# Kernel tuning notes

Measured on AMD Instinct MI355X. Metric: run time of the kernel, lower is better.

The kernel has to match this reference:

```python
import jax, jax.numpy as jnp
import numpy as np

N_NODES = 100000
N_EDGES = 600000
IN_C, HID, OUT_C = 128, 128, 64
DROPOUT_P = 0.5
BN_EPS = 1e-5


def setup_inputs() -> dict:
    key = jax.random.key(0)
    ks = jax.random.split(key, 16)
    d = {}
    d["x"] = jax.random.normal(ks[0], (N_NODES, IN_C), dtype=jnp.float32)
    d["edge_index"] = jax.random.randint(ks[1], (2, N_EDGES), 0, N_NODES, dtype=jnp.int32)
    d["norm_A"] = jax.random.uniform(ks[2], (N_EDGES,), dtype=jnp.float32)
    # GCNConv weights (glorot-ish scale) and biases
    d["W1"] = jax.random.normal(ks[3], (IN_C, HID), dtype=jnp.float32) / np.sqrt(IN_C)
    d["b1"] = jnp.zeros((HID,), dtype=jnp.float32)
    d["W2"] = jax.random.normal(ks[4], (HID, HID), dtype=jnp.float32) / np.sqrt(HID)
    d["b2"] = jnp.zeros((HID,), dtype=jnp.float32)
    d["W3"] = jax.random.normal(ks[5], (HID, HID), dtype=jnp.float32) / np.sqrt(HID)
    d["b3"] = jnp.zeros((HID,), dtype=jnp.float32)
    # BatchNorm affine params (2 BN layers for num_layers=3)
    d["g1"] = jnp.ones((HID,), dtype=jnp.float32)
    d["bt1"] = jnp.zeros((HID,), dtype=jnp.float32)
    d["g2"] = jnp.ones((HID,), dtype=jnp.float32)
    d["bt2"] = jnp.zeros((HID,), dtype=jnp.float32)
    # final projection (jk_type='max' -> Linear(HID, OUT_C))
    d["Wf"] = jax.random.normal(ks[6], (HID, OUT_C), dtype=jnp.float32) / np.sqrt(HID)
    d["bf"] = jnp.zeros((OUT_C,), dtype=jnp.float32)
    return d


def _gcn_conv(h, edge_index, ew, W, b):
    # GCNConv(cached=False, normalize=False): transform then weighted scatter-add
    h = h @ W                                   # [N, C]
    msg = ew[:, None] * h[edge_index[0]]        # gather sources, scale per-edge
    agg = jax.ops.segment_sum(msg, edge_index[1], num_segments=N_NODES)
    return agg + b


def _bn_train(h, g, bt):
    mu = jnp.mean(h, axis=0)
    var = jnp.var(h, axis=0)  # biased, as torch BN uses for normalization
    return g * (h - mu) * jax.lax.rsqrt(var + BN_EPS) + bt


def _dropout(h, key):
    keep = jax.random.bernoulli(key, 1.0 - DROPOUT_P, h.shape)
    return jnp.where(keep, h / (1.0 - DROPOUT_P), 0.0)


def reference(x, edge_index, norm_A, W1, b1, W2, b2, W3, b3, g1, bt1, g2, bt2, Wf, bf):
    dk = jax.random.key(42)
    k1, k2 = jax.random.split(dk)
    # layer 1
    h = _gcn_conv(x, edge_index, norm_A, W1, b1)
    h = jax.nn.relu(_bn_train(h, g1, bt1))
    x1 = h
    h = _dropout(h, k1)
    # layer 2
    h = _gcn_conv(h, edge_index, norm_A, W2, b2)
    h = jax.nn.relu(_bn_train(h, g2, bt2))
    x2 = h
    h = _dropout(h, k2)
    # layer 3 (no BN/relu/dropout)
    x3 = _gcn_conv(h, edge_index, norm_A, W3, b3)
    # JumpingKnowledge 'max': elementwise max over layer outputs
    jk = jnp.maximum(jnp.maximum(x1, x2), x3)
    out = jk @ Wf + bf
    return jax.nn.log_softmax(out, axis=1)
```

## Files before the change

kernel.cpp:

```cpp
#include <hip/hip_runtime.h>
#include <stdint.h>

#define N_NODES 100000
#define N_EDGES 600000
#define HID 128
#define OUT_C 64
#define NELEMS 12800000
#define BN_EPS 1e-5f
#define LP 136

typedef short bf16x8 __attribute__((ext_vector_type(8)));
typedef float f32x4 __attribute__((ext_vector_type(4)));

__device__ __forceinline__ unsigned short f2bf(float f) {
  uint32_t u = __float_as_uint(f);
  uint32_t r = u + 0x7FFFu + ((u >> 16) & 1u);
  return (unsigned short)(r >> 16);
}
__device__ __forceinline__ float bf_lo(uint32_t u) { return __uint_as_float(u << 16); }
__device__ __forceinline__ float bf_hi(uint32_t u) { return __uint_as_float(u & 0xFFFF0000u); }

__device__ __host__ __forceinline__ void threefry2x32(uint32_t k0, uint32_t k1,
                                                      uint32_t x0, uint32_t x1,
                                                      uint32_t& o0, uint32_t& o1) {
  uint32_t ks0 = k0, ks1 = k1, ks2 = k0 ^ k1 ^ 0x1BD11BDAu;
  x0 += ks0; x1 += ks1;
#define TFR(r) { x0 += x1; x1 = (x1 << (r)) | (x1 >> (32 - (r))); x1 ^= x0; }
  TFR(13) TFR(15) TFR(26) TFR(6)
  x0 += ks1; x1 += ks2 + 1u;
  TFR(17) TFR(29) TFR(16) TFR(24)
  x0 += ks2; x1 += ks0 + 2u;
  TFR(13) TFR(15) TFR(26) TFR(6)
  x0 += ks0; x1 += ks1 + 3u;
  TFR(17) TFR(29) TFR(16) TFR(24)
  x0 += ks1; x1 += ks2 + 4u;
  TFR(13) TFR(15) TFR(26) TFR(6)
  x0 += ks2; x1 += ks0 + 5u;
#undef TFR
  o0 = x0; o1 = x1;
}

__device__ __forceinline__ uint32_t jax_bits32(uint32_t k0, uint32_t k1, uint32_t i) {
  uint32_t b0, b1;
  threefry2x32(k0, k1, 0u, i, b0, b1);
  return b0 ^ b1;
}

__global__ __launch_bounds__(256) void transpose_w(const float* __restrict__ W,
                                                   int K, int C,
                                                   unsigned short* __restrict__ out) {
  int idx = blockIdx.x * 256 + threadIdx.x;
  if (idx < K * C) {
    int k = idx / C, c = idx - k * C;
    out[c * K + k] = f2bf(W[idx]);
  }
}

__device__ __forceinline__ void stage_Wt(const float* __restrict__ W,
                                         unsigned short* Wt, int tid) {
#pragma unroll
  for (int i = 0; i < 16; ++i) {
    int f4 = tid + i * 256;
    int k = f4 >> 5;
    int cq = f4 & 31;
    float4 w = *(const float4*)(W + k * 128 + cq * 4);
    Wt[(cq * 4 + 0) * LP + k] = f2bf(w.x);
    Wt[(cq * 4 + 1) * LP + k] = f2bf(w.y);
    Wt[(cq * 4 + 2) * LP + k] = f2bf(w.z);
    Wt[(cq * 4 + 3) * LP + k] = f2bf(w.w);
  }
}

__device__ __forceinline__ void mfma_compute_store(const unsigned short* At,
                                                   const unsigned short* Wt,
                                                   unsigned short* __restrict__ O,
                                                   int rbase, int tid) {
  const int lane = tid & 63;
  const int wv = tid >> 6;
  const int m = lane & 15;
  const int kg = lane >> 4;
  f32x4 acc0 = {0,0,0,0}, acc1 = {0,0,0,0}, acc2 = {0,0,0,0}, acc3 = {0,0,0,0};
  f32x4 acc4 = {0,0,0,0}, acc5 = {0,0,0,0}, acc6 = {0,0,0,0}, acc7 = {0,0,0,0};
  const unsigned short* Arow = At + (wv * 16 + m) * LP;
#pragma unroll
  for (int ks = 0; ks < 4; ++ks) {
    bf16x8 af = *(const bf16x8*)(Arow + ks * 32 + kg * 8);
#define MF(n, accn) { bf16x8 bfr = *(const bf16x8*)(Wt + (n * 16 + m) * LP + ks * 32 + kg * 8); \
    accn = __builtin_amdgcn_mfma_f32_16x16x32_bf16(af, bfr, accn, 0, 0, 0); }
    MF(0, acc0) MF(1, acc1) MF(2, acc2) MF(3, acc3)
    MF(4, acc4) MF(5, acc5) MF(6, acc6) MF(7, acc7)
#undef MF
  }
#define ST(n, accn) {                                                       \
  _Pragma("unroll")                                                         \
  for (int j = 0; j < 4; ++j) {                                             \
    int grow = rbase + wv * 16 + kg * 4 + j;                                \
    if (grow < N_NODES) O[(size_t)grow * 128 + n * 16 + m] = f2bf(accn[j]); \
  } }
  ST(0, acc0) ST(1, acc1) ST(2, acc2) ST(3, acc3)
  ST(4, acc4) ST(5, acc5) ST(6, acc6) ST(7, acc7)
#undef ST
}

__global__ __launch_bounds__(256) void gemm_mfma(const float* __restrict__ A,
                                                 const float* __restrict__ W,
                                                 unsigned short* __restrict__ O) {
  __shared__ __align__(16) unsigned short Wt[128 * LP];
  __shared__ __align__(16) unsigned short At[64 * LP];
  const int tid = threadIdx.x;
  const int rbase = blockIdx.x * 64;
  stage_Wt(W, Wt, tid);
#pragma unroll
  for (int i = 0; i < 8; ++i) {
    int f4 = tid + i * 256;
    int r = f4 >> 5;
    int cq = f4 & 31;
    int grow = rbase + r;
    if (grow >= N_NODES) grow = N_NODES - 1;
    float4 a = *(const float4*)(A + (size_t)grow * 128 + cq * 4);
    uint32_t p0 = (uint32_t)f2bf(a.x) | ((uint32_t)f2bf(a.y) << 16);
    uint32_t p1 = (uint32_t)f2bf(a.z) | ((uint32_t)f2bf(a.w) << 16);
    *(uint2*)(At + r * LP + cq * 4) = make_uint2(p0, p1);
  }
  __syncthreads();
  mfma_compute_store(At, Wt, O, rbase, tid);
}

__global__ __launch_bounds__(256) void gemm_mfma_fused(const float* __restrict__ AGG,
                                                       const float2* __restrict__ ss,
                                                       const unsigned short* __restrict__ Wt,
                                                       unsigned int* __restrict__ Xb,
                                                       unsigned short* __restrict__ O,
                                                       uint32_t k0, uint32_t k1) {
  const int tid = threadIdx.x;
  const int lane = tid & 63;
  const int wv = tid >> 6;
  const int m = lane & 15;
  const int kg = lane >> 4;
  const int rbase = blockIdx.x * 64;
  int row = rbase + wv * 16 + m;
  bool valid = row < N_NODES;
  int rowc = valid ? row : N_NODES - 1;
  const float* Ar = AGG + (size_t)rowc * 128 + kg * 8;
  bf16x8 af0, af1, af2, af3;
#define LDF(ksc, afk) {                                                        \
    float4 a0 = *(const float4*)(Ar + ksc);                                    \
    float4 a1 = *(const float4*)(Ar + ksc + 4);                                \
    const float2* ssp = ss + ksc + kg * 8;                                     \
    float av[8] = {a0.x, a0.y, a0.z, a0.w, a1.x, a1.y, a1.z, a1.w};            \
    unsigned short yb[8];                                                      \
    _Pragma("unroll")                                                          \
    for (int jj = 0; jj < 8; ++jj) {                                           \
      float2 sv = ssp[jj];                                                     \
      float yv = fmaxf(fmaf(av[jj], sv.x, sv.y), 0.f);                         \
      uint32_t bits = jax_bits32(k0, k1, (uint32_t)(rowc * 128 + ksc + kg * 8 + jj)); \
      yb[jj] = f2bf(yv);                                                       \
      afk[jj] = (short)f2bf((bits & 0x80000000u) ? 0.f : 2.f * yv);            \
    }                                                                          \
    if (valid) {                                                               \
      uint4 yp;                                                                \
      yp.x = (uint32_t)yb[0] | ((uint32_t)yb[1] << 16);                        \
      yp.y = (uint32_t)yb[2] | ((uint32_t)yb[3] << 16);                        \
      yp.z = (uint32_t)yb[4] | ((uint32_t)yb[5] << 16);                        \
      yp.w = (uint32_t)yb[6] | ((uint32_t)yb[7] << 16);                        \
      *(uint4*)(Xb + (size_t)row * 64 + (ksc) / 2 + kg * 4) = yp;              \
    } }
  LDF(0, af0) LDF(32, af1) LDF(64, af2) LDF(96, af3)
#undef LDF
  f32x4 acc0 = {0,0,0,0}, acc1 = {0,0,0,0}, acc2 = {0,0,0,0}, acc3 = {0,0,0,0};
  f32x4 acc4 = {0,0,0,0}, acc5 = {0,0,0,0}, acc6 = {0,0,0,0}, acc7 = {0,0,0,0};
  const unsigned short* Wm = Wt + m * 128 + kg * 8;
#define MFMA_ALL(afk, ksc)                                                              \
  acc0 = __builtin_amdgcn_mfma_f32_16x16x32_bf16(afk, *(const bf16x8*)(Wm + 0 * 2048 + ksc), acc0, 0, 0, 0); \
  acc1 = __builtin_amdgcn_mfma_f32_16x16x32_bf16(afk, *(const bf16x8*)(Wm + 1 * 2048 + ksc), acc1, 0, 0, 0); \
  acc2 = __builtin_amdgcn_mfma_f32_16x16x32_bf16(afk, *(const bf16x8*)(Wm + 2 * 2048 + ksc), acc2, 0, 0, 0); \
  acc3 = __builtin_amdgcn_mfma_f32_16x16x32_bf16(afk, *(const bf16x8*)(Wm + 3 * 2048 + ksc), acc3, 0, 0, 0); \
  acc4 = __builtin_amdgcn_mfma_f32_16x16x32_bf16(afk, *(const bf16x8*)(Wm + 4 * 2048 + ksc), acc4, 0, 0, 0); \
  acc5 = __builtin_amdgcn_mfma_f32_16x16x32_bf16(afk, *(const bf16x8*)(Wm + 5 * 2048 + ksc), acc5, 0, 0, 0); \
  acc6 = __builtin_amdgcn_mfma_f32_16x16x32_bf16(afk, *(const bf16x8*)(Wm + 6 * 2048 + ksc), acc6, 0, 0, 0); \
  acc7 = __builtin_amdgcn_mfma_f32_16x16x32_bf16(afk, *(const bf16x8*)(Wm + 7 * 2048 + ksc), acc7, 0, 0, 0);
  MFMA_ALL(af0, 0) MFMA_ALL(af1, 32) MFMA_ALL(af2, 64) MFMA_ALL(af3, 96)
#undef MFMA_ALL
#pragma unroll
  for (int j = 0; j < 4; ++j) {
    int orow = rbase + wv * 16 + kg * 4 + j;
    if (orow < N_NODES) {
      unsigned short* op = O + (size_t)orow * 128 + m;
      op[0 * 16] = f2bf(acc0[j]); op[1 * 16] = f2bf(acc1[j]);
      op[2 * 16] = f2bf(acc2[j]); op[3 * 16] = f2bf(acc3[j]);
      op[4 * 16] = f2bf(acc4[j]); op[5 * 16] = f2bf(acc5[j]);
      op[6 * 16] = f2bf(acc6[j]); op[7 * 16] = f2bf(acc7[j]);
    }
  }
}

__global__ __launch_bounds__(256) void csr_count(const int* __restrict__ ei,
                                                 int* __restrict__ cnt) {
  int e = blockIdx.x * 256 + threadIdx.x;
  if (e < N_EDGES) atomicAdd(&cnt[ei[e + N_EDGES]], 1);
}

__global__ __launch_bounds__(256) void scan_blocks(int* __restrict__ cnt,
                                                   int* __restrict__ bsum) {
  __shared__ int tmp[256];
  int tid = threadIdx.x;
  int i = blockIdx.x * 256 + tid;
  int v = (i < N_NODES) ? cnt[i] : 0;
  tmp[tid] = v;
  __syncthreads();
  for (int off = 1; off < 256; off <<= 1) {
    int t = (tid >= off) ? tmp[tid - off] : 0;
    __syncthreads();
    if (tid >= off) tmp[tid] += t;
    __syncthreads();
  }
  if (i < N_NODES) cnt[i] = tmp[tid] - v;
  if (tid == 255) bsum[blockIdx.x] = tmp[255];
}

__global__ __launch_bounds__(512) void scan_bsum(int* __restrict__ bsum, int nb) {
  __shared__ int tmp[512];
  int tid = threadIdx.x;
  int v = (tid < nb) ? bsum[tid] : 0;
  tmp[tid] = v;
  __syncthreads();
  for (int off = 1; off < 512; off <<= 1) {
    int t = (tid >= off) ? tmp[tid - off] : 0;
    __syncthreads();
    if (tid >= off) tmp[tid] += t;
    __syncthreads();
  }
  if (tid < nb) bsum[tid] = tmp[tid] - v;
}

__global__ __launch_bounds__(256) void add_offsets(int* __restrict__ cnt,
                                                   const int* __restrict__ bsum,
                                                   int* __restrict__ row_ptr) {
  int i = blockIdx.x * 256 + threadIdx.x;
  if (i < N_NODES) {
    int r = cnt[i] + bsum[blockIdx.x];
    row_ptr[i] = r;
    cnt[i] = r;
  }
  if (i == 0) row_ptr[N_NODES] = N_EDGES;
}

__global__ __launch_bounds__(256) void csr_fill(const int* __restrict__ ei,
                                                const float* __restrict__ ew,
                                                int* __restrict__ cursor,
                                                int2* __restrict__ edges) {
  int e = blockIdx.x * 256 + threadIdx.x;
  if (e < N_EDGES) {
    int d = ei[e + N_EDGES];
    int p = atomicAdd(&cursor[d], 1);
    edges[p] = make_int2(ei[e], __float_as_int(ew[e]));
  }
}

template <bool STATS>
__global__ __launch_bounds__(256) void gather_agg(const unsigned int* __restrict__ Hb,
                                                  const int* __restrict__ row_ptr,
                                                  const int2* __restrict__ edges,
                                                  const float* __restrict__ bias,
                                                  float* __restrict__ AGG,
                                                  float* __restrict__ partials) {
  const int hw = threadIdx.x >> 5;
  const int l32 = threadIdx.x & 31;
  const int node = blockIdx.x * 8 + hw;
  float4 acc = *(const float4*)(bias + l32 * 4);
  const int beg = row_ptr[node];
  const int end = row_ptr[node + 1];
  const unsigned int* Hp = Hb + l32 * 2;
  int j = beg;
  for (; j + 3 < end; j += 4) {
    int2 e0 = edges[j + 0];
    int2 e1 = edges[j + 1];
    int2 e2 = edges[j + 2];
    int2 e3 = edges[j + 3];
    uint2 u0 = *(const uint2*)(Hp + (size_t)e0.x * 64);
    uint2 u1 = *(const uint2*)(Hp + (size_t)e1.x * 64);
    uint2 u2 = *(const uint2*)(Hp + (size_t)e2.x * 64);
    uint2 u3 = *(const uint2*)(Hp + (size_t)e3.x * 64);
    float w0 = __int_as_float(e0.y), w1 = __int_as_float(e1.y);
    float w2 = __int_as_float(e2.y), w3 = __int_as_float(e3.y);
    acc.x += w0 * bf_lo(u0.x) + w1 * bf_lo(u1.x) + w2 * bf_lo(u2.x) + w3 * bf_lo(u3.x);
    acc.y += w0 * bf_hi(u0.x) + w1 * bf_hi(u1.x) + w2 * bf_hi(u2.x) + w3 * bf_hi(u3.x);
    acc.z += w0 * bf_lo(u0.y) + w1 * bf_lo(u1.y) + w2 * bf_lo(u2.y) + w3 * bf_lo(u3.y);
    acc.w += w0 * bf_hi(u0.y) + w1 * bf_hi(u1.y) + w2 * bf_hi(u2.y) + w3 * bf_hi(u3.y);
  }
  for (; j < end; ++j) {
    int2 e = edges[j];
    uint2 u = *(const uint2*)(Hp + (size_t)e.x * 64);
    float w = __int_as_float(e.y);
    acc.x += w * bf_lo(u.x);
    acc.y += w * bf_hi(u.x);
    acc.z += w * bf_lo(u.y);
    acc.w += w * bf_hi(u.y);
  }
  *(float4*)(AGG + (size_t)node * 128 + l32 * 4) = acc;

  if (STATS) {
    __shared__ float st[8][256];
    st[hw][l32 * 4 + 0] = acc.x;
    st[hw][l32 * 4 + 1] = acc.y;
    st[hw][l32 * 4 + 2] = acc.z;
    st[hw][l32 * 4 + 3] = acc.w;
    st[hw][128 + l32 * 4 + 0] = acc.x * acc.x;
    st[hw][128 + l32 * 4 + 1] = acc.y * acc.y;
    st[hw][128 + l32 * 4 + 2] = acc.z * acc.z;
    st[hw][128 + l32 * 4 + 3] = acc.w * acc.w;
    __syncthreads();
    float t = 0.f;
#pragma unroll
    for (int g = 0; g < 8; ++g) t += st[g][threadIdx.x];
    unsafeAtomicAdd(&partials[(blockIdx.x & 63) * 256 + threadIdx.x], t);
  }
}

__global__ __launch_bounds__(128) void stats_finalize(float* __restrict__ partials,
                                                      const float* __restrict__ g,
                                                      const float* __restrict__ bt,
                                                      float2* __restrict__ ss) {
  int c = threadIdx.x;
  float s = 0.f, q = 0.f;
#pragma unroll 8
  for (int b = 0; b < 64; ++b) {
    s += partials[b * 256 + c];
    q += partials[b * 256 + 128 + c];
  }
#pragma unroll 8
  for (int b = 0; b < 64; ++b) {
    partials[b * 256 + c] = 0.f;
    partials[b * 256 + 128 + c] = 0.f;
  }
  float mu = s * (1.0f / N_NODES);
  float var = fmaxf(q * (1.0f / N_NODES) - mu * mu, 0.f);
  float inv = rsqrtf(var + BN_EPS);
  float sc = g[c] * inv;
  ss[c] = make_float2(sc, bt[c] - mu * sc);
}

__global__ __launch_bounds__(256) void jk_final_mfma(const unsigned int* __restrict__ X1b,
                                                     const unsigned int* __restrict__ X2b,
                                                     const float* __restrict__ X3,
                                                     const float* __restrict__ Wf,
                                                     const float* __restrict__ bf,
                                                     float* __restrict__ OUT) {
  __shared__ __align__(16) unsigned short Wt[64 * LP];
  __shared__ __align__(16) unsigned short At[64 * LP];
  const int tid = threadIdx.x;
  const int rbase = blockIdx.x * 64;
#pragma unroll
  for (int i = 0; i < 8; ++i) {
    int f4 = tid + i * 256;
    int k = f4 >> 4;
    int cq = f4 & 15;
    float4 w = *(const float4*)(Wf + k * 64 + cq * 4);
    Wt[(cq * 4 + 0) * LP + k] = f2bf(w.x);
    Wt[(cq * 4 + 1) * LP + k] = f2bf(w.y);
    Wt[(cq * 4 + 2) * LP + k] = f2bf(w.z);
    Wt[(cq * 4 + 3) * LP + k] = f2bf(w.w);
  }
#pragma unroll
  for (int i = 0; i < 8; ++i) {
    int f4 = tid + i * 256;
    int r = f4 >> 5;
    int cq = f4 & 31;
    int grow = rbase + r;
    if (grow >= N_NODES) grow = N_NODES - 1;
    uint2 u1 = *(const uint2*)(X1b + (size_t)grow * 64 + cq * 2);
    uint2 u2 = *(const uint2*)(X2b + (size_t)grow * 64 + cq * 2);
    float4 x3 = *(const float4*)(X3 + (size_t)grow * 128 + cq * 4);
    float m0 = fmaxf(fmaxf(bf_lo(u1.x), bf_lo(u2.x)), x3.x);
    float m1 = fmaxf(fmaxf(bf_hi(u1.x), bf_hi(u2.x)), x3.y);
    float m2 = fmaxf(fmaxf(bf_lo(u1.y), bf_lo(u2.y)), x3.z);
    float m3 = fmaxf(fmaxf(bf_hi(u1.y), bf_hi(u2.y)), x3.w);
    uint32_t p0 = (uint32_t)f2bf(m0) | ((uint32_t)f2bf(m1) << 16);
    uint32_t p1 = (uint32_t)f2bf(m2) | ((uint32_t)f2bf(m3) << 16);
    *(uint2*)(At + r * LP + cq * 4) = make_uint2(p0, p1);
  }
  __syncthreads();
  const int lane = tid & 63;
  const int wv = tid >> 6;
  const int m = lane & 15;
  const int kg = lane >> 4;
  f32x4 acc0 = {0,0,0,0}, acc1 = {0,0,0,0}, acc2 = {0,0,0,0}, acc3 = {0,0,0,0};
  const unsigned short* Arow = At + (wv * 16 + m) * LP;
#pragma unroll
  for (int ks = 0; ks < 4; ++ks) {
    bf16x8 af = *(const bf16x8*)(Arow + ks * 32 + kg * 8);
#define MF(n, accn) { bf16x8 bfr = *(const bf16x8*)(Wt + (n * 16 + m) * LP + ks * 32 + kg * 8); \
    accn = __builtin_amdgcn_mfma_f32_16x16x32_bf16(af, bfr, accn, 0, 0, 0); }
    MF(0, acc0) MF(1, acc1) MF(2, acc2) MF(3, acc3)
#undef MF
  }
  float bf0 = bf[m], bf1 = bf[16 + m], bf2 = bf[32 + m], bf3 = bf[48 + m];
#pragma unroll
  for (int j = 0; j < 4; ++j) {
    int row = rbase + wv * 16 + kg * 4 + j;
    float v0 = acc0[j] + bf0;
    float v1 = acc1[j] + bf1;
    float v2 = acc2[j] + bf2;
    float v3 = acc3[j] + bf3;
    float M = fmaxf(fmaxf(v0, v1), fmaxf(v2, v3));
#pragma unroll
    for (int s = 1; s < 16; s <<= 1) M = fmaxf(M, __shfl_xor(M, s));
    float sum = expf(v0 - M) + expf(v1 - M) + expf(v2 - M) + expf(v3 - M);
#pragma unroll
    for (int s = 1; s < 16; s <<= 1) sum += __shfl_xor(sum, s);
    float ls = M + logf(sum);
    if (row < N_NODES) {
      float* o = OUT + (size_t)row * 64;
      o[m] = v0 - ls;
      o[16 + m] = v1 - ls;
      o[32 + m] = v2 - ls;
      o[48 + m] = v3 - ls;
    }
  }
}

extern "C" void kernel_launch(void* const* d_in, const int* in_sizes, int n_in,
                              void* d_out, int out_size, void* d_ws, size_t ws_size,
                              hipStream_t stream) {
  const float* x   = (const float*)d_in[0];
  const int*   ei  = (const int*)d_in[1];
  const float* ew  = (const float*)d_in[2];
  const float* W1  = (const float*)d_in[3];
  const float* b1  = (const float*)d_in[4];
  const float* W2  = (const float*)d_in[5];
  const float* b2  = (const float*)d_in[6];
  const float* W3  = (const float*)d_in[7];
  const float* b3  = (const float*)d_in[8];
  const float* g1  = (const float*)d_in[9];
  const float* bt1 = (const float*)d_in[10];
  const float* g2  = (const float*)d_in[11];
  const float* bt2 = (const float*)d_in[12];
  const float* Wf  = (const float*)d_in[13];
  const float* bfb = (const float*)d_in[14];
  float* out = (float*)d_out;

  float* B0 = (float*)d_ws;
  float* B1 = B0 + NELEMS;
  float* B2 = B1 + NELEMS;
  float* B3 = B2 + NELEMS;
  int2* edges = (int2*)(B3 + NELEMS);
  int* cursor = (int*)(edges + N_EDGES);
  int* row_ptr = cursor + N_NODES;
  int* bsum = row_ptr + N_NODES + 1;
  float* partials = (float*)(bsum + 512);
  float2* ss1 = (float2*)(partials + 64 * 256);
  float2* ss2 = ss1 + 128;
  unsigned short* Wt2 = (unsigned short*)(ss2 + 128);
  unsigned short* Wt3 = Wt2 + 128 * 128;
  unsigned short* P = (unsigned short*)B0;
  unsigned int* Pu = (unsigned int*)B0;
  unsigned int* X1b = (unsigned int*)B2;
  unsigned int* X2b = (unsigned int*)B3;

  uint32_t k1_0, k1_1, k2_0, k2_1;
  threefry2x32(0u, 42u, 0u, 0u, k1_0, k1_1);
  threefry2x32(0u, 42u, 0u, 1u, k2_0, k2_1);

  const int GEMM_GRID = (N_NODES + 63) / 64;
  const int EDGE_GRID = (N_EDGES + 255) / 256;
  const int NODE_GRID = (N_NODES + 255) / 256;
  const int AGG_GRID  = N_NODES / 8;
  const int FINAL_GRID = (N_NODES + 63) / 64;
  const int TR_GRID = (128 * 128 + 255) / 256;

  transpose_w<<<TR_GRID, 256, 0, stream>>>(W2, 128, 128, Wt2);
  transpose_w<<<TR_GRID, 256, 0, stream>>>(W3, 128, 128, Wt3);
  hipMemsetAsync(cursor, 0, N_NODES * sizeof(int), stream);
  hipMemsetAsync(partials, 0, 64 * 256 * sizeof(float), stream);
  csr_count<<<EDGE_GRID, 256, 0, stream>>>(ei, cursor);
  scan_blocks<<<NODE_GRID, 256, 0, stream>>>(cursor, bsum);
  scan_bsum<<<1, 512, 0, stream>>>(bsum, NODE_GRID);
  add_offsets<<<NODE_GRID, 256, 0, stream>>>(cursor, bsum, row_ptr);
  csr_fill<<<EDGE_GRID, 256, 0, stream>>>(ei, ew, cursor, edges);

  gemm_mfma<<<GEMM_GRID, 256, 0, stream>>>(x, W1, P);
  gather_agg<true><<<AGG_GRID, 256, 0, stream>>>(Pu, row_ptr, edges, b1, B1, partials);
  stats_finalize<<<1, 128, 0, stream>>>(partials, g1, bt1, ss1);
  gemm_mfma_fused<<<GEMM_GRID, 256, 0, stream>>>(B1, ss1, Wt2, X1b, P, k1_0, k1_1);
  gather_agg<true><<<AGG_GRID, 256, 0, stream>>>(Pu, row_ptr, edges, b2, B1, partials);
  stats_finalize<<<1, 128, 0, stream>>>(partials, g2, bt2, ss2);
  gemm_mfma_fused<<<GEMM_GRID, 256, 0, stream>>>(B1, ss2, Wt3, X2b, P, k2_0, k2_1);
  gather_agg<false><<<AGG_GRID, 256, 0, stream>>>(Pu, row_ptr, edges, b3, B1, nullptr);
  jk_final_mfma<<<FINAL_GRID, 256, 0, stream>>>(X1b, X2b, B1, Wf, bfb, out);
}
```

Before: 352.7 us.

## Fold BN stats finalize into fused GEMM and store layer-3 aggregate as bf16

```diff
diff --git a/kernel.cpp b/kernel.cpp
--- a/kernel.cpp
+++ b/kernel.cpp
@@ -46,14 +46,16 @@
   return b0 ^ b1;
 }
 
-__global__ __launch_bounds__(256) void transpose_w(const float* __restrict__ W,
-                                                   int K, int C,
-                                                   unsigned short* __restrict__ out) {
+__global__ __launch_bounds__(256) void transpose_w23(const float* __restrict__ W2,
+                                                     const float* __restrict__ W3,
+                                                     unsigned short* __restrict__ Wt2,
+                                                     unsigned short* __restrict__ Wt3) {
   int idx = blockIdx.x * 256 + threadIdx.x;
-  if (idx < K * C) {
-    int k = idx / C, c = idx - k * C;
-    out[c * K + k] = f2bf(W[idx]);
-  }
+  const float* W = (idx < 16384) ? W2 : W3;
+  unsigned short* out = (idx < 16384) ? Wt2 : Wt3;
+  int e = idx & 16383;
+  int k = e >> 7, c = e & 127;
+  out[c * 128 + k] = f2bf(W[e]);
 }
 
 __device__ __forceinline__ void stage_Wt(const float* __restrict__ W,
@@ -127,12 +129,32 @@
 }
 
 __global__ __launch_bounds__(256) void gemm_mfma_fused(const float* __restrict__ AGG,
-                                                       const float2* __restrict__ ss,
+                                                       const float* __restrict__ partials,
+                                                       const float* __restrict__ g,
+                                                       const float* __restrict__ bt,
                                                        const unsigned short* __restrict__ Wt,
                                                        unsigned int* __restrict__ Xb,
                                                        unsigned short* __restrict__ O,
                                                        uint32_t k0, uint32_t k1) {
   const int tid = threadIdx.x;
+  __shared__ float red[256];
+  __shared__ float2 ssl[128];
+  {
+    float t0 = 0.f;
+#pragma unroll 8
+    for (int b = 0; b < 64; ++b) t0 += partials[b * 256 + tid];
+    red[tid] = t0;
+    __syncthreads();
+    if (tid < 128) {
+      float s = red[tid], q = red[128 + tid];
+      float mu = s * (1.0f / N_NODES);
+      float var = fmaxf(q * (1.0f / N_NODES) - mu * mu, 0.f);
+      float inv = rsqrtf(var + BN_EPS);
+      float sc = g[tid] * inv;
+      ssl[tid] = make_float2(sc, bt[tid] - mu * sc);
+    }
+    __syncthreads();
+  }
   const int lane = tid & 63;
   const int wv = tid >> 6;
   const int m = lane & 15;
@@ -146,7 +168,7 @@
 #define LDF(ksc, afk) {                                                        \
     float4 a0 = *(const float4*)(Ar + ksc);                                    \
     float4 a1 = *(const float4*)(Ar + ksc + 4);                                \
-    const float2* ssp = ss + ksc + kg * 8;                                     \
+    const float2* ssp = ssl + ksc + kg * 8;                                    \
     float av[8] = {a0.x, a0.y, a0.z, a0.w, a1.x, a1.y, a1.z, a1.w};            \
     unsigned short yb[8];                                                      \
     _Pragma("unroll")                                                          \
@@ -262,7 +284,8 @@
                                                   const int* __restrict__ row_ptr,
                                                   const int2* __restrict__ edges,
                                                   const float* __restrict__ bias,
-                                                  float* __restrict__ AGG,
+                                                  float* __restrict__ AGGf,
+                                                  unsigned int* __restrict__ AGGb,
                                                   float* __restrict__ partials) {
   const int hw = threadIdx.x >> 5;
   const int l32 = threadIdx.x & 31;
@@ -297,9 +320,8 @@
     acc.z += w * bf_lo(u.y);
     acc.w += w * bf_hi(u.y);
   }
-  *(float4*)(AGG + (size_t)node * 128 + l32 * 4) = acc;
-
   if (STATS) {
+    *(float4*)(AGGf + (size_t)node * 128 + l32 * 4) = acc;
     __shared__ float st[8][256];
     st[hw][l32 * 4 + 0] = acc.x;
     st[hw][l32 * 4 + 1] = acc.y;
@@ -314,35 +336,17 @@
 #pragma unroll
     for (int g = 0; g < 8; ++g) t += st[g][threadIdx.x];
     unsafeAtomicAdd(&partials[(blockIdx.x & 63) * 256 + threadIdx.x], t);
-  }
-}
-
-__global__ __launch_bounds__(128) void stats_finalize(float* __restrict__ partials,
-                                                      const float* __restrict__ g,
-                                                      const float* __restrict__ bt,
-                                                      float2* __restrict__ ss) {
-  int c = threadIdx.x;
-  float s = 0.f, q = 0.f;
-#pragma unroll 8
-  for (int b = 0; b < 64; ++b) {
-    s += partials[b * 256 + c];
-    q += partials[b * 256 + 128 + c];
-  }
-#pragma unroll 8
-  for (int b = 0; b < 64; ++b) {
-    partials[b * 256 + c] = 0.f;
-    partials[b * 256 + 128 + c] = 0.f;
-  }
-  float mu = s * (1.0f / N_NODES);
-  float var = fmaxf(q * (1.0f / N_NODES) - mu * mu, 0.f);
-  float inv = rsqrtf(var + BN_EPS);
-  float sc = g[c] * inv;
-  ss[c] = make_float2(sc, bt[c] - mu * sc);
+  } else {
+    uint2 p;
+    p.x = (uint32_t)f2bf(acc.x) | ((uint32_t)f2bf(acc.y) << 16);
+    p.y = (uint32_t)f2bf(acc.z) | ((uint32_t)f2bf(acc.w) << 16);
+    *(uint2*)(AGGb + (size_t)node * 64 + l32 * 2) = p;
+  }
 }
 
 __global__ __launch_bounds__(256) void jk_final_mfma(const unsigned int* __restrict__ X1b,
                                                      const unsigned int* __restrict__ X2b,
-                                                     const float* __restrict__ X3,
+                                                     const unsigned int* __restrict__ X3b,
                                                      const float* __restrict__ Wf,
                                                      const float* __restrict__ bf,
                                                      float* __restrict__ OUT) {
@@ -370,11 +374,11 @@
     if (grow >= N_NODES) grow = N_NODES - 1;
     uint2 u1 = *(const uint2*)(X1b + (size_t)grow * 64 + cq * 2);
     uint2 u2 = *(const uint2*)(X2b + (size_t)grow * 64 + cq * 2);
-    float4 x3 = *(const float4*)(X3 + (size_t)grow * 128 + cq * 4);
-    float m0 = fmaxf(fmaxf(bf_lo(u1.x), bf_lo(u2.x)), x3.x);
-    float m1 = fmaxf(fmaxf(bf_hi(u1.x), bf_hi(u2.x)), x3.y);
-    float m2 = fmaxf(fmaxf(bf_lo(u1.y), bf_lo(u2.y)), x3.z);
-    float m3 = fmaxf(fmaxf(bf_hi(u1.y), bf_hi(u2.y)), x3.w);
+    uint2 u3 = *(const uint2*)(X3b + (size_t)grow * 64 + cq * 2);
+    float m0 = fmaxf(fmaxf(bf_lo(u1.x), bf_lo(u2.x)), bf_lo(u3.x));
+    float m1 = fmaxf(fmaxf(bf_hi(u1.x), bf_hi(u2.x)), bf_hi(u3.x));
+    float m2 = fmaxf(fmaxf(bf_lo(u1.y), bf_lo(u2.y)), bf_lo(u3.y));
+    float m3 = fmaxf(fmaxf(bf_hi(u1.y), bf_hi(u2.y)), bf_hi(u3.y));
     uint32_t p0 = (uint32_t)f2bf(m0) | ((uint32_t)f2bf(m1) << 16);
     uint32_t p1 = (uint32_t)f2bf(m2) | ((uint32_t)f2bf(m3) << 16);
     *(uint2*)(At + r * LP + cq * 4) = make_uint2(p0, p1);
@@ -445,17 +449,17 @@
   float* B3 = B2 + NELEMS;
   int2* edges = (int2*)(B3 + NELEMS);
   int* cursor = (int*)(edges + N_EDGES);
-  int* row_ptr = cursor + N_NODES;
+  float* part1 = (float*)(cursor + N_NODES);
+  float* part2 = part1 + 64 * 256;
+  int* row_ptr = (int*)(part2 + 64 * 256);
   int* bsum = row_ptr + N_NODES + 1;
-  float* partials = (float*)(bsum + 512);
-  float2* ss1 = (float2*)(partials + 64 * 256);
-  float2* ss2 = ss1 + 128;
-  unsigned short* Wt2 = (unsigned short*)(ss2 + 128);
+  unsigned short* Wt2 = (unsigned short*)(bsum + 512);
   unsigned short* Wt3 = Wt2 + 128 * 128;
   unsigned short* P = (unsigned short*)B0;
   unsigned int* Pu = (unsigned int*)B0;
   unsigned int* X1b = (unsigned int*)B2;
   unsigned int* X2b = (unsigned int*)B3;
+  unsigned int* AGG3b = (unsigned int*)B1;
 
   uint32_t k1_0, k1_1, k2_0, k2_1;
   threefry2x32(0u, 42u, 0u, 0u, k1_0, k1_1);
@@ -466,12 +470,10 @@
   const int NODE_GRID = (N_NODES + 255) / 256;
   const int AGG_GRID  = N_NODES / 8;
   const int FINAL_GRID = (N_NODES + 63) / 64;
-  const int TR_GRID = (128 * 128 + 255) / 256;
-
-  transpose_w<<<TR_GRID, 256, 0, stream>>>(W2, 128, 128, Wt2);
-  transpose_w<<<TR_GRID, 256, 0, stream>>>(W3, 128, 128, Wt3);
-  hipMemsetAsync(cursor, 0, N_NODES * sizeof(int), stream);
-  hipMemsetAsync(partials, 0, 64 * 256 * sizeof(float), stream);
+  const int TR_GRID = (2 * 128 * 128 + 255) / 256;
+
+  transpose_w23<<<TR_GRID, 256, 0, stream>>>(W2, W3, Wt2, Wt3);
+  hipMemsetAsync(cursor, 0, N_NODES * sizeof(int) + 2 * 64 * 256 * sizeof(float), stream);
   csr_count<<<EDGE_GRID, 256, 0, stream>>>(ei, cursor);
   scan_blocks<<<NODE_GRID, 256, 0, stream>>>(cursor, bsum);
   scan_bsum<<<1, 512, 0, stream>>>(bsum, NODE_GRID);
@@ -479,12 +481,10 @@
   csr_fill<<<EDGE_GRID, 256, 0, stream>>>(ei, ew, cursor, edges);
 
   gemm_mfma<<<GEMM_GRID, 256, 0, stream>>>(x, W1, P);
-  gather_agg<true><<<AGG_GRID, 256, 0, stream>>>(Pu, row_ptr, edges, b1, B1, partials);
-  stats_finalize<<<1, 128, 0, stream>>>(partials, g1, bt1, ss1);
-  gemm_mfma_fused<<<GEMM_GRID, 256, 0, stream>>>(B1, ss1, Wt2, X1b, P, k1_0, k1_1);
-  gather_agg<true><<<AGG_GRID, 256, 0, stream>>>(Pu, row_ptr, edges, b2, B1, partials);
-  stats_finalize<<<1, 128, 0, stream>>>(partials, g2, bt2, ss2);
-  gemm_mfma_fused<<<GEMM_GRID, 256, 0, stream>>>(B1, ss2, Wt3, X2b, P, k2_0, k2_1);
-  gather_agg<false><<<AGG_GRID, 256, 0, stream>>>(Pu, row_ptr, edges, b3, B1, nullptr);
-  jk_final_mfma<<<FINAL_GRID, 256, 0, stream>>>(X1b, X2b, B1, Wf, bfb, out);
-}
+  gather_agg<true><<<AGG_GRID, 256, 0, stream>>>(Pu, row_ptr, edges, b1, B1, nullptr, part1);
+  gemm_mfma_fused<<<GEMM_GRID, 256, 0, stream>>>(B1, part1, g1, bt1, Wt2, X1b, P, k1_0, k1_1);
+  gather_agg<true><<<AGG_GRID, 256, 0, stream>>>(Pu, row_ptr, edges, b2, B1, nullptr, part2);
+  gemm_mfma_fused<<<GEMM_GRID, 256, 0, stream>>>(B1, part2, g2, bt2, Wt3, X2b, P, k2_0, k2_1);
+  gather_agg<false><<<AGG_GRID, 256, 0, stream>>>(Pu, row_ptr, edges, b3, nullptr, AGG3b, nullptr);
+  jk_final_mfma<<<FINAL_GRID, 256, 0, stream>>>(X1b, X2b, AGG3b, Wf, bfb, out);
+}
```

Result: faster. 340.0 us (-3.6%).
